# Optimization experiments

Measured on AMD Instinct MI355X. Metric: run time of the kernel, lower is better.

## Reference

```python
import jax, jax.numpy as jnp
import numpy as np

B, S, D, H = 2, 2048, 1024, 16
HD = D // H            # head_dim = 64
CHUNK = 1024           # hard-coded in the torch module
ROPE_THETA = 10000.0


def setup_inputs() -> dict:
    key = jax.random.key(0)
    ks = jax.random.split(key, 5)
    hidden_states = jax.random.normal(ks[0], (B, S, D), dtype=jnp.float32)
    # Precomputed RoPE frequencies: freqs_cis[s, j] = exp(i * s * theta_j),
    # stored as real [S, HD//2, 2] = (cos, sin).
    inv_freq = 1.0 / (ROPE_THETA ** (np.arange(0, HD, 2, dtype=np.float32) / HD))
    ang = np.outer(np.arange(S, dtype=np.float32), inv_freq)  # [S, HD//2]
    freqs_cis = jnp.stack([jnp.cos(ang), jnp.sin(ang)], axis=-1).astype(jnp.float32)
    scale = 0.02
    Wq = jax.random.normal(ks[1], (D, D), dtype=jnp.float32) * scale
    Wk = jax.random.normal(ks[2], (D, D), dtype=jnp.float32) * scale
    Wv = jax.random.normal(ks[3], (D, D), dtype=jnp.float32) * scale
    Wo = jax.random.normal(ks[4], (D, D), dtype=jnp.float32) * scale
    return {"hidden_states": hidden_states, "freqs_cis": freqs_cis,
            "Wq": Wq, "Wk": Wk, "Wv": Wv, "Wo": Wo}


def _apply_rope(x, freqs_cis):
    # x: [B, S, H, HD]; freqs_cis: [S, HD//2, 2] (cos, sin)
    b, s, h, hd = x.shape
    xr = x.reshape(b, s, h, hd // 2, 2)
    a, bb = xr[..., 0], xr[..., 1]
    c = freqs_cis[:s, :, 0][None, :, None, :]  # broadcast over batch, heads
    d = freqs_cis[:s, :, 1][None, :, None, :]
    # complex multiply (a + ib)(c + id)
    out = jnp.stack([a * c - bb * d, a * d + bb * c], axis=-1)
    return out.reshape(b, s, h, hd)


def reference(hidden_states, freqs_cis, Wq, Wk, Wv, Wo):
    b, s, dm = hidden_states.shape
    q = (hidden_states @ Wq).reshape(b, s, H, HD)
    k = (hidden_states @ Wk).reshape(b, s, H, HD)
    v = (hidden_states @ Wv).reshape(b, s, H, HD)
    q = _apply_rope(q, freqs_cis)
    k = _apply_rope(k, freqs_cis)
    q = q.transpose(0, 2, 1, 3)  # [B, H, S, HD]
    k = k.transpose(0, 2, 1, 3)
    v = v.transpose(0, 2, 1, 3)
    scaling = HD ** (-0.5)
    out = jnp.zeros_like(q)
    # Faithful replication of the (buggy) chunked attention: softmax is
    # normalized PER key-chunk, then chunk outputs are summed.
    for i in range(0, s, CHUNK):
        j = min(i + CHUNK, s)
        w = jnp.einsum('bhqd,bhkd->bhqk', q, k[:, :, i:j]) * scaling
        w = jax.nn.softmax(w.astype(jnp.float32), axis=-1).astype(q.dtype)
        out = out + jnp.einsum('bhqk,bhkd->bhqd', w, v[:, :, i:j])
    out = out.transpose(0, 2, 1, 3).reshape(b, s, dm)
    return out @ Wo
```

## Files before the change

### kernel.cpp

```cpp
#include <hip/hip_runtime.h>
#include <hip/hip_bf16.h>
#include <cstdint>

typedef __bf16 bf16x8 __attribute__((ext_vector_type(8)));
typedef float f32x4 __attribute__((ext_vector_type(4)));
typedef float f32x16 __attribute__((ext_vector_type(16)));

#define MFMA16(a, b, c) __builtin_amdgcn_mfma_f32_16x16x32_bf16(a, b, c, 0, 0, 0)
#define MFMA32(a, b, c) __builtin_amdgcn_mfma_f32_32x32x16_bf16(a, b, c, 0, 0, 0)

__device__ __forceinline__ void gload_lds16(const void* g, void* l) {
  __builtin_amdgcn_global_load_lds(
      (const __attribute__((address_space(1))) unsigned int*)g,
      (__attribute__((address_space(3))) unsigned int*)l, 16, 0, 0);
}

__device__ __forceinline__ unsigned short f2bf(float x) {
  union { float f; uint32_t u; } v; v.f = x;
  uint32_t r = v.u + 0x7fff + ((v.u >> 16) & 1);
  return (unsigned short)(r >> 16);
}
__device__ __forceinline__ float bf2f(unsigned short h) {
  union { float f; uint32_t u; } v; v.u = ((uint32_t)h) << 16;
  return v.f;
}
__device__ __forceinline__ f32x16 fzero16() {
  f32x16 v;
#pragma unroll
  for (int i = 0; i < 16; ++i) v[i] = 0.f;
  return v;
}

__device__ __forceinline__ void ptrans(const f32x16& sv, float& rsum,
                                       bf16x8& f0, bf16x8& f1) {
  float ps[16];
#pragma unroll
  for (int r = 0; r < 16; ++r) ps[r] = __builtin_exp2f(sv[r]);
  float rs = 0.f;
#pragma unroll
  for (int r = 0; r < 16; ++r) rs += ps[r];
  rsum += rs;
  bf16x8 a, b;
#pragma unroll
  for (int r = 0; r < 8; ++r) a[r] = (__bf16)ps[r];
#pragma unroll
  for (int r = 0; r < 8; ++r) b[r] = (__bf16)ps[8 + r];
  f0 = a; f1 = b;
}

__global__ __launch_bounds__(256) void k_split(const float* __restrict__ x,
                                               unsigned short* __restrict__ hi, int n4) {
  int i = blockIdx.x * blockDim.x + threadIdx.x;
  if (i >= n4) return;
  float4 v = ((const float4*)x)[i];
  ushort4 h;
  h.x = f2bf(v.x); h.y = f2bf(v.y); h.z = f2bf(v.z); h.w = f2bf(v.w);
  ((ushort4*)hi)[i] = h;
}

__global__ __launch_bounds__(256) void k_wsplit(
    const float* __restrict__ Wq, const float* __restrict__ Wk,
    const float* __restrict__ Wv, const float* __restrict__ Wo,
    unsigned short* __restrict__ WtqH, unsigned short* __restrict__ WtkH,
    unsigned short* __restrict__ WtvH, unsigned short* __restrict__ WtoH) {
  const int z = blockIdx.z;
  const float* W = (z == 0) ? Wq : (z == 1) ? Wk : (z == 2) ? Wv : Wo;
  unsigned short* WtH = (z == 0) ? WtqH : (z == 1) ? WtkH : (z == 2) ? WtvH : WtoH;
  __shared__ float tile[32][33];
  const int bx = blockIdx.x, by = blockIdx.y;
  const int tx = threadIdx.x & 31, ty = threadIdx.x >> 5;
#pragma unroll
  for (int i = 0; i < 4; ++i)
    tile[ty + i * 8][tx] = W[(size_t)(by * 32 + ty + i * 8) * 1024 + bx * 32 + tx];
  __syncthreads();
#pragma unroll
  for (int i = 0; i < 4; ++i) {
    float v = tile[tx][ty + i * 8];
    WtH[(size_t)(bx * 32 + ty + i * 8) * 1024 + by * 32 + tx] = f2bf(v);
  }
}

__global__ __launch_bounds__(256, 2) void k_qkv(
    const unsigned short* __restrict__ hsH,
    const unsigned short* __restrict__ WqH, const unsigned short* __restrict__ WkH,
    const unsigned short* __restrict__ WvH, const float* __restrict__ freqs,
    unsigned short* __restrict__ qB, unsigned short* __restrict__ kB,
    unsigned short* __restrict__ vB) {
  __shared__ unsigned short Ah[128 * 32], Bh[128 * 32];
  const int tid = threadIdx.x;
  const int bm = blockIdx.y, bn = blockIdx.x;
  const int w = bn >> 3;
  const int n0 = (bn & 7) * 128;
  const unsigned short* WH = (w == 0) ? WqH : (w == 1) ? WkH : WvH;
  const int lane = tid & 63, wave = tid >> 6;
  const int wm = (wave & 1) * 64, wn = (wave >> 1) * 64;
  const int l15 = lane & 15, lq = lane >> 4;

  f32x4 acc[4][4];
#pragma unroll
  for (int i = 0; i < 4; i++)
#pragma unroll
    for (int j = 0; j < 4; j++) acc[i][j] = (f32x4){0.f, 0.f, 0.f, 0.f};

  const char* baseA = (const char*)hsH + (size_t)(bm * 128) * 2048;
  const char* baseB = (const char*)WH + (size_t)n0 * 2048;
  const int off0 = tid << 4, row0 = off0 >> 6, seg0 = off0 & 63;
  const int off1 = (tid + 256) << 4, row1 = off1 >> 6, seg1 = off1 & 63;

  for (int k0 = 0; k0 < 1024; k0 += 32) {
    __syncthreads();
    gload_lds16(baseA + (size_t)row0 * 2048 + k0 * 2 + seg0, (char*)Ah + wave * 1024);
    gload_lds16(baseB + (size_t)row0 * 2048 + k0 * 2 + seg0, (char*)Bh + wave * 1024);
    gload_lds16(baseA + (size_t)row1 * 2048 + k0 * 2 + seg1,
                (char*)Ah + 4096 + wave * 1024);
    gload_lds16(baseB + (size_t)row1 * 2048 + k0 * 2 + seg1,
                (char*)Bh + 4096 + wave * 1024);
    __syncthreads();
    bf16x8 ah[4], bh[4];
#pragma unroll
    for (int i = 0; i < 4; ++i) {
      ah[i] = *(const bf16x8*)&Ah[(wm + i * 16 + l15) * 32 + lq * 8];
      bh[i] = *(const bf16x8*)&Bh[(wn + i * 16 + l15) * 32 + lq * 8];
    }
#pragma unroll
    for (int i = 0; i < 4; ++i)
#pragma unroll
      for (int j = 0; j < 4; ++j) acc[i][j] = MFMA16(ah[i], bh[j], acc[i][j]);
  }

  unsigned short* dst = (w == 0) ? qB : (w == 1) ? kB : vB;
#pragma unroll
  for (int i = 0; i < 4; ++i) {
#pragma unroll
    for (int j = 0; j < 4; ++j) {
      int colw = n0 + wn + j * 16 + l15;
      int h = colw >> 6, d = colw & 63;
#pragma unroll
      for (int r = 0; r < 4; ++r) {
        int rowg = bm * 128 + wm + i * 16 + lq * 4 + r;
        int s = rowg & 2047, b = rowg >> 11;
        float val = acc[i][j][r];
        if (w < 2) {
          float partner = __shfl_xor(val, 1);
          int jj = d >> 1;
          float cs = freqs[(s * 32 + jj) * 2 + 0];
          float sn = freqs[(s * 32 + jj) * 2 + 1];
          float res = (d & 1) ? (partner * sn + val * cs) : (val * cs - partner * sn);
          if (w == 0) res *= 0.18033688011112042f;
          dst[(((size_t)(b * 16 + h)) * 2048 + s) * 64 + d] = f2bf(res);
        } else {
          int sp = (s & ~12) | ((s & 4) << 1) | ((s & 8) >> 1);
          dst[(((size_t)(b * 16 + h)) * 64 + d) * 2048 + sp] = f2bf(val);
        }
      }
    }
  }
}

__global__ __launch_bounds__(256, 2) void k_attn(
    const unsigned short* __restrict__ qB, const unsigned short* __restrict__ kB,
    const unsigned short* __restrict__ vB,
    unsigned short* __restrict__ c0, unsigned short* __restrict__ c1) {
  const int tid = threadIdx.x, lane = tid & 63, wave = tid >> 6;
  const int l31 = lane & 31, lh = lane >> 5;
  const int bid = blockIdx.x;
  const int x = (bid >> 3) & 7;
  const int gg = (bid & 7) + 8 * (bid >> 6);
  const int bh = gg & 31;
  const int chunk = gg >> 5;
  const int q0 = x * 256 + wave * 64;
  const size_t base = (size_t)bh * 2048 * 64;

  bf16x8 qf[2][4];
#pragma unroll
  for (int qt = 0; qt < 2; ++qt)
#pragma unroll
    for (int ks = 0; ks < 4; ++ks)
      qf[qt][ks] = *(const bf16x8*)(qB + base + (size_t)(q0 + qt * 32 + l31) * 64 +
                                    ks * 16 + lh * 8);

  const unsigned short* kp = kB + base + (size_t)chunk * 1024 * 64 + l31 * 64 + lh * 8;
  const unsigned short* vp = vB + base + l31 * 2048 + chunk * 1024 + lh * 8;

  bf16x8 kfa[4], kfb[4];
#pragma unroll
  for (int ks = 0; ks < 4; ++ks) {
    kfa[ks] = *(const bf16x8*)(kp + ks * 16);
    kfb[ks] = *(const bf16x8*)(kp + 2048 + ks * 16);
  }
  kp += 4096;

  f32x16 o[2][2];
#pragma unroll
  for (int a = 0; a < 2; ++a)
#pragma unroll
    for (int bq = 0; bq < 2; ++bq) o[a][bq] = fzero16();
  float rsum[2] = {0.f, 0.f};

  for (int kb = 0; kb < 16; ++kb) {
    bf16x8 vf[2][4];
#pragma unroll
    for (int dt = 0; dt < 2; ++dt)
#pragma unroll
      for (int ks = 0; ks < 4; ++ks)
        vf[dt][ks] = *(const bf16x8*)(vp + dt * 65536 + ks * 16);

    bf16x8 f0, f1;
    {
      f32x16 s0 = fzero16(), s1 = fzero16();
#pragma unroll
      for (int ks = 0; ks < 4; ++ks) {
        s0 = MFMA32(kfa[ks], qf[0][ks], s0);
        s1 = MFMA32(kfa[ks], qf[1][ks], s1);
      }
#pragma unroll
      for (int ks = 0; ks < 4; ++ks) kfa[ks] = *(const bf16x8*)(kp + ks * 16);
      ptrans(s0, rsum[0], f0, f1);
      o[0][0] = MFMA32(vf[0][0], f0, o[0][0]);
      o[1][0] = MFMA32(vf[1][0], f0, o[1][0]);
      o[0][0] = MFMA32(vf[0][1], f1, o[0][0]);
      o[1][0] = MFMA32(vf[1][1], f1, o[1][0]);
      ptrans(s1, rsum[1], f0, f1);
      o[0][1] = MFMA32(vf[0][0], f0, o[0][1]);
      o[1][1] = MFMA32(vf[1][0], f0, o[1][1]);
      o[0][1] = MFMA32(vf[0][1], f1, o[0][1]);
      o[1][1] = MFMA32(vf[1][1], f1, o[1][1]);
    }
    {
      f32x16 s0 = fzero16(), s1 = fzero16();
#pragma unroll
      for (int ks = 0; ks < 4; ++ks) {
        s0 = MFMA32(kfb[ks], qf[0][ks], s0);
        s1 = MFMA32(kfb[ks], qf[1][ks], s1);
      }
#pragma unroll
      for (int ks = 0; ks < 4; ++ks)
        kfb[ks] = *(const bf16x8*)(kp + 2048 + ks * 16);
      ptrans(s0, rsum[0], f0, f1);
      o[0][0] = MFMA32(vf[0][2], f0, o[0][0]);
      o[1][0] = MFMA32(vf[1][2], f0, o[1][0]);
      o[0][0] = MFMA32(vf[0][3], f1, o[0][0]);
      o[1][0] = MFMA32(vf[1][3], f1, o[1][0]);
      ptrans(s1, rsum[1], f0, f1);
      o[0][1] = MFMA32(vf[0][2], f0, o[0][1]);
      o[1][1] = MFMA32(vf[1][2], f0, o[1][1]);
      o[0][1] = MFMA32(vf[0][3], f1, o[0][1]);
      o[1][1] = MFMA32(vf[1][3], f1, o[1][1]);
    }
    kp += 4096;
    vp += 64;
  }

  unsigned short* cB = chunk ? c1 : c0;
  const int b = bh >> 4, h = bh & 15;
#pragma unroll
  for (int qt = 0; qt < 2; ++qt) {
    float lsum = rsum[qt] + __shfl_xor(rsum[qt], 32);
    float inv = 1.f / lsum;
    int s = q0 + qt * 32 + l31;
#pragma unroll
    for (int dt = 0; dt < 2; ++dt)
#pragma unroll
      for (int g = 0; g < 4; ++g) {
        int d = dt * 32 + 4 * lh + 8 * g;
        size_t idx = ((size_t)(b * 2048 + s)) * 1024 + h * 64 + d;
        ushort4 hv;
#pragma unroll
        for (int t = 0; t < 4; ++t)
          ((unsigned short*)&hv)[t] = f2bf(o[dt][qt][g * 4 + t] * inv);
        *(ushort4*)(cB + idx) = hv;
      }
  }
}

__global__ __launch_bounds__(256) void k_comb(const unsigned short* __restrict__ c0,
                                              const unsigned short* __restrict__ c1,
                                              unsigned short* __restrict__ outB,
                                              int n8) {
  int i = blockIdx.x * blockDim.x + threadIdx.x;
  if (i >= n8) return;
  uint4 a = ((const uint4*)c0)[i];
  uint4 b = ((const uint4*)c1)[i];
  uint4 r;
  const unsigned short* pa = (const unsigned short*)&a;
  const unsigned short* pb = (const unsigned short*)&b;
  unsigned short* pr = (unsigned short*)&r;
#pragma unroll
  for (int j = 0; j < 8; ++j) pr[j] = f2bf(bf2f(pa[j]) + bf2f(pb[j]));
  ((uint4*)outB)[i] = r;
}

__global__ __launch_bounds__(256, 2) void k_out(const unsigned short* __restrict__ A,
                                                const unsigned short* __restrict__ B,
                                                float* __restrict__ out) {
  __shared__ unsigned short Ah[128 * 32], Bh[128 * 32];
  const int tid = threadIdx.x;
  const int bm = blockIdx.y, n0 = blockIdx.x * 128;
  const int lane = tid & 63, wave = tid >> 6;
  const int wm = (wave & 1) * 64, wn = (wave >> 1) * 64;
  const int l15 = lane & 15, lq = lane >> 4;

  f32x4 acc[4][4];
#pragma unroll
  for (int i = 0; i < 4; i++)
#pragma unroll
    for (int j = 0; j < 4; j++) acc[i][j] = (f32x4){0.f, 0.f, 0.f, 0.f};

  const char* baseA = (const char*)A + (size_t)(bm * 128) * 2048;
  const char* baseB = (const char*)B + (size_t)n0 * 2048;
  const int off0 = tid << 4, row0 = off0 >> 6, seg0 = off0 & 63;
  const int off1 = (tid + 256) << 4, row1 = off1 >> 6, seg1 = off1 & 63;

  for (int k0 = 0; k0 < 1024; k0 += 32) {
    __syncthreads();
    gload_lds16(baseA + (size_t)row0 * 2048 + k0 * 2 + seg0, (char*)Ah + wave * 1024);
    gload_lds16(baseB + (size_t)row0 * 2048 + k0 * 2 + seg0, (char*)Bh + wave * 1024);
    gload_lds16(baseA + (size_t)row1 * 2048 + k0 * 2 + seg1,
                (char*)Ah + 4096 + wave * 1024);
    gload_lds16(baseB + (size_t)row1 * 2048 + k0 * 2 + seg1,
                (char*)Bh + 4096 + wave * 1024);
    __syncthreads();
    bf16x8 ah[4], bh[4];
#pragma unroll
    for (int i = 0; i < 4; ++i) {
      ah[i] = *(const bf16x8*)&Ah[(wm + i * 16 + l15) * 32 + lq * 8];
      bh[i] = *(const bf16x8*)&Bh[(wn + i * 16 + l15) * 32 + lq * 8];
    }
#pragma unroll
    for (int i = 0; i < 4; ++i)
#pragma unroll
      for (int j = 0; j < 4; ++j) acc[i][j] = MFMA16(ah[i], bh[j], acc[i][j]);
  }
#pragma unroll
  for (int i = 0; i < 4; ++i)
#pragma unroll
    for (int j = 0; j < 4; ++j) {
      int colw = n0 + wn + j * 16 + l15;
#pragma unroll
      for (int r = 0; r < 4; ++r) {
        int rowg = bm * 128 + wm + i * 16 + lq * 4 + r;
        out[(size_t)rowg * 1024 + colw] = acc[i][j][r];
      }
    }
}

extern "C" void kernel_launch(void* const* d_in, const int* in_sizes, int n_in,
                              void* d_out, int out_size, void* d_ws, size_t ws_size,
                              hipStream_t stream) {
  const float* hs = (const float*)d_in[0];
  const float* freqs = (const float*)d_in[1];
  const float* Wq = (const float*)d_in[2];
  const float* Wk = (const float*)d_in[3];
  const float* Wv = (const float*)d_in[4];
  const float* Wo = (const float*)d_in[5];
  float* out = (float*)d_out;

  const size_t MD = (size_t)4096 * 1024;
  const size_t WW = (size_t)1024 * 1024;
  unsigned short* hsH = (unsigned short*)d_ws;
  unsigned short* WtqH = hsH + MD;
  unsigned short* WtkH = WtqH + WW;
  unsigned short* WtvH = WtkH + WW;
  unsigned short* WtoH = WtvH + WW;
  unsigned short* qB = WtoH + WW;
  unsigned short* kB = qB + MD;
  unsigned short* vB = kB + MD;
  unsigned short* c0 = vB + MD;
  unsigned short* c1 = c0 + MD;
  unsigned short* attnB = hsH;

  k_split<<<4096, 256, 0, stream>>>(hs, hsH, (int)(MD / 4));
  k_wsplit<<<dim3(32, 32, 4), 256, 0, stream>>>(Wq, Wk, Wv, Wo,
                                                WtqH, WtkH, WtvH, WtoH);
  k_qkv<<<dim3(24, 32), 256, 0, stream>>>(hsH, WtqH, WtkH, WtvH, freqs, qB, kB, vB);
  k_attn<<<512, 256, 0, stream>>>(qB, kB, vB, c0, c1);
  k_comb<<<2048, 256, 0, stream>>>(c0, c1, attnB, (int)(MD / 8));
  k_out<<<dim3(8, 32), 256, 0, stream>>>(attnB, WtoH, out);
}
```

Measured before the change: 243.6 us.

## Split attention key chunks into halves and defer softmax normalization to combine

Each 1024-key chunk is now split into two 512-key halves, doubling the attention grid to 1024 blocks, and occupancy is raised to 4 blocks per SM. The attention kernel stores unnormalized partial outputs plus row sums, and the combine kernel sums the halves and divides by the chunk sums. The aim is better GPU fill and latency hiding for an under-occupied attention kernel. Wave priority is also raised around MFMA sections. The cost is more intermediate traffic (four bf16 partials plus sums) and some extra bf16 rounding of unnormalized values.

```diff
diff --git a/kernel.cpp b/kernel.cpp
--- a/kernel.cpp
+++ b/kernel.cpp
@@ -157,18 +157,22 @@
   }
 }
 
-__global__ __launch_bounds__(256, 2) void k_attn(
+__global__ __launch_bounds__(256, 4) void k_attn(
     const unsigned short* __restrict__ qB, const unsigned short* __restrict__ kB,
     const unsigned short* __restrict__ vB,
-    unsigned short* __restrict__ c0, unsigned short* __restrict__ c1) {
+    unsigned short* __restrict__ p00, unsigned short* __restrict__ p01,
+    unsigned short* __restrict__ p10, unsigned short* __restrict__ p11,
+    float* __restrict__ rsB) {
   const int tid = threadIdx.x, lane = tid & 63, wave = tid >> 6;
   const int l31 = lane & 31, lh = lane >> 5;
   const int bid = blockIdx.x;
   const int x = (bid >> 3) & 7;
   const int gg = (bid & 7) + 8 * (bid >> 6);
   const int bh = gg & 31;
-  const int chunk = gg >> 5;
+  const int chunk = (gg >> 5) & 1;
+  const int sub = gg >> 6;
   const int q0 = x * 256 + wave * 64;
+  const int key0 = chunk * 1024 + sub * 512;
   const size_t base = (size_t)bh * 2048 * 64;
 
   bf16x8 qf[2][4];
@@ -179,8 +183,8 @@
       qf[qt][ks] = *(const bf16x8*)(qB + base + (size_t)(q0 + qt * 32 + l31) * 64 +
                                     ks * 16 + lh * 8);
 
-  const unsigned short* kp = kB + base + (size_t)chunk * 1024 * 64 + l31 * 64 + lh * 8;
-  const unsigned short* vp = vB + base + l31 * 2048 + chunk * 1024 + lh * 8;
+  const unsigned short* kp = kB + base + (size_t)key0 * 64 + l31 * 64 + lh * 8;
+  const unsigned short* vp = vB + base + l31 * 2048 + key0 + lh * 8;
 
   bf16x8 kfa[4], kfb[4];
 #pragma unroll
@@ -197,7 +201,7 @@
     for (int bq = 0; bq < 2; ++bq) o[a][bq] = fzero16();
   float rsum[2] = {0.f, 0.f};
 
-  for (int kb = 0; kb < 16; ++kb) {
+  for (int kb = 0; kb < 8; ++kb) {
     bf16x8 vf[2][4];
 #pragma unroll
     for (int dt = 0; dt < 2; ++dt)
@@ -208,56 +212,69 @@
     bf16x8 f0, f1;
     {
       f32x16 s0 = fzero16(), s1 = fzero16();
+      __builtin_amdgcn_s_setprio(1);
 #pragma unroll
       for (int ks = 0; ks < 4; ++ks) {
         s0 = MFMA32(kfa[ks], qf[0][ks], s0);
         s1 = MFMA32(kfa[ks], qf[1][ks], s1);
       }
+      __builtin_amdgcn_s_setprio(0);
 #pragma unroll
       for (int ks = 0; ks < 4; ++ks) kfa[ks] = *(const bf16x8*)(kp + ks * 16);
       ptrans(s0, rsum[0], f0, f1);
+      __builtin_amdgcn_s_setprio(1);
       o[0][0] = MFMA32(vf[0][0], f0, o[0][0]);
       o[1][0] = MFMA32(vf[1][0], f0, o[1][0]);
       o[0][0] = MFMA32(vf[0][1], f1, o[0][0]);
       o[1][0] = MFMA32(vf[1][1], f1, o[1][0]);
+      __builtin_amdgcn_s_setprio(0);
       ptrans(s1, rsum[1], f0, f1);
+      __builtin_amdgcn_s_setprio(1);
       o[0][1] = MFMA32(vf[0][0], f0, o[0][1]);
       o[1][1] = MFMA32(vf[1][0], f0, o[1][1]);
       o[0][1] = MFMA32(vf[0][1], f1, o[0][1]);
       o[1][1] = MFMA32(vf[1][1], f1, o[1][1]);
+      __builtin_amdgcn_s_setprio(0);
     }
     {
       f32x16 s0 = fzero16(), s1 = fzero16();
+      __builtin_amdgcn_s_setprio(1);
 #pragma unroll
       for (int ks = 0; ks < 4; ++ks) {
         s0 = MFMA32(kfb[ks], qf[0][ks], s0);
         s1 = MFMA32(kfb[ks], qf[1][ks], s1);
       }
+      __builtin_amdgcn_s_setprio(0);
 #pragma unroll
       for (int ks = 0; ks < 4; ++ks)
         kfb[ks] = *(const bf16x8*)(kp + 2048 + ks * 16);
       ptrans(s0, rsum[0], f0, f1);
+      __builtin_amdgcn_s_setprio(1);
       o[0][0] = MFMA32(vf[0][2], f0, o[0][0]);
       o[1][0] = MFMA32(vf[1][2], f0, o[1][0]);
       o[0][0] = MFMA32(vf[0][3], f1, o[0][0]);
       o[1][0] = MFMA32(vf[1][3], f1, o[1][0]);
+      __builtin_amdgcn_s_setprio(0);
       ptrans(s1, rsum[1], f0, f1);
+      __builtin_amdgcn_s_setprio(1);
       o[0][1] = MFMA32(vf[0][2], f0, o[0][1]);
       o[1][1] = MFMA32(vf[1][2], f0, o[1][1]);
       o[0][1] = MFMA32(vf[0][3], f1, o[0][1]);
       o[1][1] = MFMA32(vf[1][3], f1, o[1][1]);
+      __builtin_amdgcn_s_setprio(0);
     }
     kp += 4096;
     vp += 64;
   }
 
-  unsigned short* cB = chunk ? c1 : c0;
+  unsigned short* pB = chunk ? (sub ? p11 : p10) : (sub ? p01 : p00);
+  float* rsp = rsB + (size_t)(chunk * 2 + sub) * 65536 + (size_t)bh * 2048;
   const int b = bh >> 4, h = bh & 15;
 #pragma unroll
   for (int qt = 0; qt < 2; ++qt) {
     float lsum = rsum[qt] + __shfl_xor(rsum[qt], 32);
-    float inv = 1.f / lsum;
     int s = q0 + qt * 32 + l31;
+    if (lh == 0) rsp[s] = lsum;
 #pragma unroll
     for (int dt = 0; dt < 2; ++dt)
 #pragma unroll
@@ -267,26 +284,39 @@
         ushort4 hv;
 #pragma unroll
         for (int t = 0; t < 4; ++t)
-          ((unsigned short*)&hv)[t] = f2bf(o[dt][qt][g * 4 + t] * inv);
-        *(ushort4*)(cB + idx) = hv;
+          ((unsigned short*)&hv)[t] = f2bf(o[dt][qt][g * 4 + t]);
+        *(ushort4*)(pB + idx) = hv;
       }
   }
 }
 
-__global__ __launch_bounds__(256) void k_comb(const unsigned short* __restrict__ c0,
-                                              const unsigned short* __restrict__ c1,
-                                              unsigned short* __restrict__ outB,
-                                              int n8) {
+__global__ __launch_bounds__(256) void k_comb(
+    const unsigned short* __restrict__ p00, const unsigned short* __restrict__ p01,
+    const unsigned short* __restrict__ p10, const unsigned short* __restrict__ p11,
+    const float* __restrict__ rsB, unsigned short* __restrict__ outB, int n8) {
   int i = blockIdx.x * blockDim.x + threadIdx.x;
   if (i >= n8) return;
-  uint4 a = ((const uint4*)c0)[i];
-  uint4 b = ((const uint4*)c1)[i];
+  int flat = i << 3;
+  int b = flat >> 21;
+  int s = (flat >> 10) & 2047;
+  int h = (flat >> 6) & 15;
+  int bhq = (b * 16 + h) * 2048 + s;
+  float inv0 = 1.f / (rsB[bhq] + rsB[65536 + bhq]);
+  float inv1 = 1.f / (rsB[131072 + bhq] + rsB[196608 + bhq]);
+  uint4 a0 = ((const uint4*)p00)[i];
+  uint4 a1 = ((const uint4*)p01)[i];
+  uint4 b0 = ((const uint4*)p10)[i];
+  uint4 b1 = ((const uint4*)p11)[i];
   uint4 r;
-  const unsigned short* pa = (const unsigned short*)&a;
-  const unsigned short* pb = (const unsigned short*)&b;
+  const unsigned short* qa0 = (const unsigned short*)&a0;
+  const unsigned short* qa1 = (const unsigned short*)&a1;
+  const unsigned short* qb0 = (const unsigned short*)&b0;
+  const unsigned short* qb1 = (const unsigned short*)&b1;
   unsigned short* pr = (unsigned short*)&r;
 #pragma unroll
-  for (int j = 0; j < 8; ++j) pr[j] = f2bf(bf2f(pa[j]) + bf2f(pb[j]));
+  for (int j = 0; j < 8; ++j)
+    pr[j] = f2bf((bf2f(qa0[j]) + bf2f(qa1[j])) * inv0 +
+                 (bf2f(qb0[j]) + bf2f(qb1[j])) * inv1);
   ((uint4*)outB)[i] = r;
 }
 
@@ -365,15 +395,18 @@
   unsigned short* qB = WtoH + WW;
   unsigned short* kB = qB + MD;
   unsigned short* vB = kB + MD;
-  unsigned short* c0 = vB + MD;
-  unsigned short* c1 = c0 + MD;
-  unsigned short* attnB = hsH;
+  unsigned short* p00 = vB + MD;
+  unsigned short* p01 = p00 + MD;
+  unsigned short* p11 = p01 + MD;
+  float* rsB = (float*)(p11 + MD);
+  unsigned short* p10 = hsH;
+  unsigned short* attnB = qB;
 
   k_split<<<4096, 256, 0, stream>>>(hs, hsH, (int)(MD / 4));
   k_wsplit<<<dim3(32, 32, 4), 256, 0, stream>>>(Wq, Wk, Wv, Wo,
                                                 WtqH, WtkH, WtvH, WtoH);
   k_qkv<<<dim3(24, 32), 256, 0, stream>>>(hsH, WtqH, WtkH, WtvH, freqs, qB, kB, vB);
-  k_attn<<<512, 256, 0, stream>>>(qB, kB, vB, c0, c1);
-  k_comb<<<2048, 256, 0, stream>>>(c0, c1, attnB, (int)(MD / 8));
+  k_attn<<<1024, 256, 0, stream>>>(qB, kB, vB, p00, p01, p10, p11, rsB);
+  k_comb<<<2048, 256, 0, stream>>>(p00, p01, p10, p11, rsB, attnB, (int)(MD / 8));
   k_out<<<dim3(8, 32), 256, 0, stream>>>(attnB, WtoH, out);
 }
```

After: 666.4 us. +173.5%, slower.
